# Optimization experiments

Hardware: AMD Instinct MI355X
Metric: run time of the kernel (lower is better)

Reference implementation:

```python
import jax, jax.numpy as jnp
import numpy as np

B, N, P, K, E = 4, 20000, 128, 128, 160000


def setup_inputs() -> dict:
    key = jax.random.key(0)
    ks = jax.random.split(key, 16)
    inv_p = 1.0 / np.sqrt(P)
    inv_3p = 1.0 / np.sqrt(3 * P)
    return {
        "x_in": jax.random.normal(ks[0], (B, N, P), jnp.float32),
        "vertex_areas": jax.random.uniform(ks[1], (B, N), jnp.float32, 1e-3, 1.0),
        "evals": jax.random.uniform(ks[2], (B, K), jnp.float32, 0.0, 10.0),
        "evecs": jax.random.normal(ks[3], (B, N, K), jnp.float32),
        "gradX_vals": jax.random.normal(ks[4], (B, E), jnp.float32),
        "gradY_vals": jax.random.normal(ks[5], (B, E), jnp.float32),
        "grad_rows": jax.random.randint(ks[6], (B, E), 0, N, jnp.int32),
        "grad_cols": jax.random.randint(ks[7], (B, E), 0, N, jnp.int32),
        # learned params
        "diffusion_times": jax.random.uniform(ks[8], (P,), jnp.float32, 1e-3, 0.1),
        "B_re": jax.random.normal(ks[9], (P, P), jnp.float32) * inv_p,
        "B_im": jax.random.normal(ks[10], (P, P), jnp.float32) * inv_p,
        "W1": jax.random.normal(ks[11], (P, 3 * P), jnp.float32) * inv_3p,
        "b1": jnp.zeros((P,), jnp.float32),
        "W2": jax.random.normal(ks[12], (P, P), jnp.float32) * inv_p,
        "b2": jnp.zeros((P,), jnp.float32),
        "W3": jax.random.normal(ks[13], (P, P), jnp.float32) * inv_p,
        "b3": jnp.zeros((P,), jnp.float32),
    }


def _spmm(rows, cols, vals, x):
    # sparse (n,n) @ dense (n,p) via COO gather/scatter
    return jax.ops.segment_sum(vals[:, None] * x[cols], rows, num_segments=x.shape[0])


def reference(x_in, vertex_areas, evals, evecs, gradX_vals, gradY_vals,
              grad_rows, grad_cols, diffusion_times, B_re, B_im,
              W1, b1, W2, b2, W3, b3):
    # SpectralDiffusion: project -> spectral heat scaling -> unproject
    times = jnp.clip(diffusion_times, 1e-8)                       # (P,)
    x_spec = jnp.einsum('bnk,bnp->bkp', evecs, x_in * vertex_areas[..., None])
    scale = jnp.exp(-evals[..., None] * times[None, None, :])     # (B,K,P)
    x_diffuse = jnp.einsum('bnk,bkp->bnp', evecs, scale * x_spec)  # (B,N,P)

    # sparse gradient halves
    gx = jax.vmap(_spmm)(grad_rows, grad_cols, gradX_vals, x_diffuse)  # (B,N,P)
    gy = jax.vmap(_spmm)(grad_rows, grad_cols, gradY_vals, x_diffuse)

    # SpatialGradient: tanh(re*B_re(re) + im*B_im(im))
    x_grad_features = jnp.tanh(gx * (gx @ B_re.T) + gy * (gy @ B_im.T))

    # MiniMLP on concatenated features (dropout inactive in eval)
    h = jnp.concatenate([x_in, x_diffuse, x_grad_features], axis=-1)  # (B,N,3P)
    h = jax.nn.relu(h @ W1.T + b1)
    h = jax.nn.relu(h @ W2.T + b2)
    h = h @ W3.T + b3
    return h + x_in
```

## Files before the change

### kernel.cpp

```cpp
#include <hip/hip_runtime.h>
#include <hip/hip_bf16.h>
#include <cstddef>

#define B_ 4
#define N_ 20000
#define P_ 128
#define K_ 128
#define E_ 160000

constexpr int NCH_S = 79;
constexpr int NSCB  = 79;

typedef __attribute__((ext_vector_type(8))) short short8;
typedef __attribute__((ext_vector_type(4))) float f32x4;

__device__ __forceinline__ unsigned pk2(float x, float y) {
  __hip_bfloat162 h = __float22bfloat162_rn(make_float2(x, y));
  union { __hip_bfloat162 h; unsigned u; } c; c.h = h; return c.u;
}
__device__ __forceinline__ float bf2f(short s) {
  union { unsigned u; float f; } c; c.u = ((unsigned)(unsigned short)s) << 16; return c.f;
}
__device__ __forceinline__ short f2bs(float x) {
  union { __hip_bfloat16 h; short s; } c; c.h = __float2bfloat16(x); return c.s;
}

__global__ __launch_bounds__(256)
void k_prep(const float* __restrict__ ev, const float* __restrict__ xin,
            const float* __restrict__ areas,
            __hip_bfloat16* __restrict__ evT, __hip_bfloat16* __restrict__ xT)
{
  const int tn = blockIdx.x, half = blockIdx.y & 1, mat = blockIdx.y >> 1;
  const int b = blockIdx.z, t = threadIdx.x;
  const int n0 = tn * 64, c0 = half * 64;
  __shared__ float ld[64][65];
  const float* src = (mat ? xin : ev) + (size_t)b * N_ * 128;
  const float* ab  = areas + (size_t)b * N_;
#pragma unroll
  for (int i = 0; i < 4; ++i) {
    int gid = t + i * 256;
    int r = gid >> 4, c4 = (gid & 15) << 2;
    int n = n0 + r;
    float4 v = make_float4(0.f, 0.f, 0.f, 0.f);
    if (n < N_) {
      v = *(const float4*)(src + (size_t)n * 128 + c0 + c4);
      if (mat == 0) { float ar = ab[n]; v.x *= ar; v.y *= ar; v.z *= ar; v.w *= ar; }
    }
    ld[r][c4] = v.x; ld[r][c4+1] = v.y; ld[r][c4+2] = v.z; ld[r][c4+3] = v.w;
  }
  __syncthreads();
  __hip_bfloat16* dst = (mat ? xT : evT) + (size_t)b * 128 * N_;
#pragma unroll
  for (int i = 0; i < 4; ++i) {
    int gid = t + i * 256;
    int cr = gid >> 4, nq = (gid & 15) << 2;
    int n = n0 + nq;
    if (n + 4 <= N_) {
      uint2 u;
      u.x = pk2(ld[nq][cr],   ld[nq+1][cr]);
      u.y = pk2(ld[nq+2][cr], ld[nq+3][cr]);
      *(uint2*)(dst + (size_t)(c0 + cr) * N_ + n) = u;
    }
  }
}

__global__ __launch_bounds__(256)
void k_wprep(const float* __restrict__ Bre, const float* __restrict__ Bim,
             uint4* __restrict__ WfRe, uint4* __restrict__ WfIm)
{
  int fid = blockIdx.x * 256 + threadIdx.x;
  if (fid >= 2048) return;
  int gg = fid >> 7, rr = fid & 127;
  const float* s0 = Bre + rr * 128 + gg * 8;
  const float* s1 = Bim + rr * 128 + gg * 8;
  float4 a0 = *(const float4*)s0, a1 = *(const float4*)(s0 + 4);
  uint4 u; u.x = pk2(a0.x, a0.y); u.y = pk2(a0.z, a0.w);
  u.z = pk2(a1.x, a1.y); u.w = pk2(a1.z, a1.w);
  WfRe[fid] = u;
  float4 b0 = *(const float4*)s1, b1 = *(const float4*)(s1 + 4);
  uint4 v; v.x = pk2(b0.x, b0.y); v.y = pk2(b0.z, b0.w);
  v.z = pk2(b1.x, b1.y); v.w = pk2(b1.z, b1.w);
  WfIm[fid] = v;
}

__device__ __forceinline__ void stg64(uint4* __restrict__ Ls,
                                      const __hip_bfloat16* __restrict__ G,
                                      int n0, int t)
{
#pragma unroll
  for (int i = 0; i < 2; ++i) {
    int gid = t + i * 512;
    int r = gid >> 3, kg = gid & 7;
    int n = n0 + kg * 8;
    uint4 u = make_uint4(0u, 0u, 0u, 0u);
    if (n < N_) u = *(const uint4*)(G + (size_t)r * N_ + n);
    Ls[r * 8 + (kg ^ (r & 7))] = u;
  }
}

__global__ __launch_bounds__(512)
void k_spec_mm(const __hip_bfloat16* __restrict__ evT,
               const __hip_bfloat16* __restrict__ xT,
               float* __restrict__ part)
{
  const int c = blockIdx.x, b = blockIdx.y, t = threadIdx.x;
  const int l = t & 63, wid = t >> 6;
  const int wr = wid >> 2, wc = wid & 3;
  const int lr = l & 15, lg = l >> 4;
  __shared__ uint4 AsB[1024];
  __shared__ uint4 WsB[1024];
  f32x4 acc[4][2];
#pragma unroll
  for (int m = 0; m < 4; ++m)
#pragma unroll
    for (int n = 0; n < 2; ++n) acc[m][n] = (f32x4)0.f;

  const __hip_bfloat16* eb = evT + (size_t)b * 128 * N_;
  const __hip_bfloat16* xb = xT  + (size_t)b * 128 * N_;

  for (int s = 0; s < 4; ++s) {
    int n0 = c * 256 + s * 64;
    __syncthreads();
    stg64(AsB, eb, n0, t);
    stg64(WsB, xb, n0, t);
    __syncthreads();
    const short8* Ap = (const short8*)AsB;
    const short8* Wp = (const short8*)WsB;
#pragma unroll
    for (int kk = 0; kk < 2; ++kk) {
      int gg = kk * 4 + lg;
      short8 a[4], w[2];
#pragma unroll
      for (int m = 0; m < 4; ++m) { int rr = wr*64 + m*16 + lr; a[m] = Ap[rr*8 + (gg ^ (rr & 7))]; }
#pragma unroll
      for (int n = 0; n < 2; ++n) { int rr = wc*32 + n*16 + lr; w[n] = Wp[rr*8 + (gg ^ (rr & 7))]; }
#pragma unroll
      for (int m = 0; m < 4; ++m)
#pragma unroll
        for (int n = 0; n < 2; ++n)
          acc[m][n] = __builtin_amdgcn_mfma_f32_16x16x32_bf16(a[m], w[n], acc[m][n], 0, 0, 0);
    }
  }

  float* po = part + ((size_t)(b * NCH_S + c) << 14);
#pragma unroll
  for (int m = 0; m < 4; ++m)
#pragma unroll
    for (int r = 0; r < 4; ++r) {
      int row = wr*64 + m*16 + lg*4 + r;
#pragma unroll
      for (int n = 0; n < 2; ++n) {
        int col = wc*32 + n*16 + lr;
        po[row * 128 + col] = acc[m][n][r];
      }
    }
}

__global__ __launch_bounds__(256)
void k_spec_reduce(const float* __restrict__ partial, const float* __restrict__ evals,
                   const float* __restrict__ times, float* __restrict__ sspecT)
{
  int idx = blockIdx.x * 256 + threadIdx.x;
  int b = idx >> 14;
  int kp = idx & 16383;
  int k = kp >> 7, p = kp & 127;
  float s = 0.f;
  const float* pb = partial + (size_t)b * NCH_S * (K_*P_) + kp;
  for (int c = 0; c < NCH_S; ++c) s += pb[(size_t)c * (K_*P_)];
  float tt = times[p]; tt = tt < 1e-8f ? 1e-8f : tt;
  float sc = __expf(-evals[b*K_ + k] * tt);
  sspecT[((size_t)b*P_ + p) * K_ + k] = s * sc;
}

__device__ __forceinline__ void stg_f32(uint4* __restrict__ Ls, const float* __restrict__ G,
                                        int ld, int nrows, int t)
{
#pragma unroll
  for (int i = 0; i < 4; ++i) {
    int gid = t + i * 512;
    int r = gid >> 4, kg = gid & 15;
    float4 v0 = make_float4(0.f,0.f,0.f,0.f), v1 = v0;
    if (r < nrows) {
      const float* p = G + (size_t)r * ld + kg * 8;
      v0 = *(const float4*)p;
      v1 = *(const float4*)(p + 4);
    }
    uint4 u;
    u.x = pk2(v0.x, v0.y); u.y = pk2(v0.z, v0.w);
    u.z = pk2(v1.x, v1.y); u.w = pk2(v1.z, v1.w);
    Ls[r * 16 + (kg ^ (r & 7))] = u;
  }
}

__device__ __forceinline__ void stg_bf(uint4* __restrict__ Ls,
                                       const __hip_bfloat16* __restrict__ G,
                                       int ld, int nrows, int t)
{
#pragma unroll
  for (int i = 0; i < 4; ++i) {
    int gid = t + i * 512;
    int r = gid >> 4, kg = gid & 15;
    uint4 u = make_uint4(0u,0u,0u,0u);
    if (r < nrows) u = *(const uint4*)(G + (size_t)r * ld + kg * 8);
    Ls[r * 16 + (kg ^ (r & 7))] = u;
  }
}

__device__ __forceinline__ void mfma_chunk(const uint4* AsB, const uint4* WsB,
                                           int wr, int wc, int lr, int lg,
                                           f32x4 acc[4][2])
{
  const short8* Ap = (const short8*)AsB;
  const short8* Wp = (const short8*)WsB;
#pragma unroll
  for (int kk = 0; kk < 4; ++kk) {
    int gg = kk * 4 + lg;
    short8 a[4], w[2];
#pragma unroll
    for (int m = 0; m < 4; ++m) {
      int rr = wr*64 + m*16 + lr;
      a[m] = Ap[rr*16 + (gg ^ (rr & 7))];
    }
#pragma unroll
    for (int n = 0; n < 2; ++n) {
      int rr = wc*32 + n*16 + lr;
      w[n] = Wp[rr*16 + (gg ^ (rr & 7))];
    }
#pragma unroll
    for (int m = 0; m < 4; ++m)
#pragma unroll
      for (int n = 0; n < 2; ++n)
        acc[m][n] = __builtin_amdgcn_mfma_f32_16x16x32_bf16(a[m], w[n], acc[m][n], 0, 0, 0);
  }
}

template<int MODE>
__global__ __launch_bounds__(512)
void k_rowgemm(const void* __restrict__ A0, const void* __restrict__ A1,
               const void* __restrict__ A2, int abf,
               const float* __restrict__ W, int ldw, int wbs, int nchunk,
               const float* __restrict__ bias, const float* __restrict__ resid,
               void* __restrict__ C)
{
  const int b = blockIdx.y, r0 = blockIdx.x * 128, t = threadIdx.x;
  const int l = t & 63, wid = t >> 6;
  const int wr = wid >> 2, wc = wid & 3;
  const int lr = l & 15, lg = l >> 4;
  __shared__ uint4 AsB[2048];
  __shared__ uint4 WsB[2048];
  f32x4 acc[4][2];
#pragma unroll
  for (int m = 0; m < 4; ++m)
#pragma unroll
    for (int n = 0; n < 2; ++n) acc[m][n] = (f32x4)0.f;

  const float* Wb = W + (size_t)b * wbs;
  const int nrows = min(128, N_ - r0);
  const size_t aoff = (size_t)b * N_ * 128 + (size_t)r0 * 128;

  for (int kc = 0; kc < nchunk; ++kc) {
    const void* Av = (kc == 0 ? A0 : (kc == 1 ? A1 : A2));
    __syncthreads();
    if ((abf >> kc) & 1) stg_bf(AsB, (const __hip_bfloat16*)Av + aoff, 128, nrows, t);
    else                 stg_f32(AsB, (const float*)Av + aoff, 128, nrows, t);
    stg_f32(WsB, Wb + kc * 128, ldw, 128, t);
    __syncthreads();
    mfma_chunk(AsB, WsB, wr, wc, lr, lg, acc);
  }

  const size_t cb = (size_t)b * N_ * 128;
#pragma unroll
  for (int m = 0; m < 4; ++m) {
    int rowt = wr*64 + m*16 + lg*4;
#pragma unroll
    for (int r = 0; r < 4; ++r) {
      int row = r0 + rowt + r;
      if (row >= N_) continue;
#pragma unroll
      for (int n = 0; n < 2; ++n) {
        int col = wc*32 + n*16 + lr;
        float v = acc[m][n][r];
        if (MODE == 1 || MODE == 2) v = fmaxf(v + bias[col], 0.f);
        if (MODE == 3) {
          v += bias[col] + resid[cb + (size_t)row*128 + col];
          ((float*)C)[cb + (size_t)row*128 + col] = v;
        } else {
          ((__hip_bfloat16*)C)[cb + (size_t)row*128 + col] = __float2bfloat16(v);
        }
      }
    }
  }
}

__device__ __forceinline__ void stg64r(uint4* __restrict__ Ls,
                                       const __hip_bfloat16* __restrict__ G,
                                       int nrows, int t)
{
#pragma unroll
  for (int i = 0; i < 4; ++i) {
    int gid = t + i * 256;
    int r = gid >> 4, kg = gid & 15;
    uint4 u = make_uint4(0u,0u,0u,0u);
    if (r < nrows) u = *(const uint4*)(G + (size_t)r * 128 + kg * 8);
    Ls[r * 16 + (kg ^ (r & 7))] = u;
  }
}

__device__ __forceinline__ void mfma_pass64(const uint4* As, const uint4* __restrict__ Wf,
                                            int wc, int lr, int lg, f32x4 acc[4][2])
{
  const short8* Ap = (const short8*)As;
  const short8* Wp = (const short8*)Wf;
#pragma unroll
  for (int kk = 0; kk < 4; ++kk) {
    int gg = kk * 4 + lg;
    short8 a[4], w[2];
#pragma unroll
    for (int m = 0; m < 4; ++m) { int rr = m*16 + lr; a[m] = Ap[rr*16 + (gg ^ (rr & 7))]; }
#pragma unroll
    for (int n = 0; n < 2; ++n) { int rr = wc*32 + n*16 + lr; w[n] = Wp[(gg << 7) + rr]; }
#pragma unroll
    for (int m = 0; m < 4; ++m)
#pragma unroll
      for (int n = 0; n < 2; ++n)
        acc[m][n] = __builtin_amdgcn_mfma_f32_16x16x32_bf16(a[m], w[n], acc[m][n], 0, 0, 0);
  }
}

__global__ __launch_bounds__(256)
void k_grad(const uint4* __restrict__ WfRe, const uint4* __restrict__ WfIm,
            __hip_bfloat16* __restrict__ gx, const __hip_bfloat16* __restrict__ gy)
{
  const int b = blockIdx.y, r0 = blockIdx.x * 64, t = threadIdx.x;
  const int l = t & 63, wc = t >> 6;
  const int lr = l & 15, lg = l >> 4;
  __shared__ uint4 As[1024];
  __shared__ uint4 As2[1024];
  f32x4 acc1[4][2], acc2[4][2];
#pragma unroll
  for (int m = 0; m < 4; ++m)
#pragma unroll
    for (int n = 0; n < 2; ++n) { acc1[m][n] = (f32x4)0.f; acc2[m][n] = (f32x4)0.f; }

  __hip_bfloat16*       gxb = gx + (size_t)b * N_ * P_;
  const __hip_bfloat16* gyb = gy + (size_t)b * N_ * P_;
  const int nrows = min(64, N_ - r0);

  stg64r(As,  gxb + (size_t)r0 * 128, nrows, t);
  stg64r(As2, gyb + (size_t)r0 * 128, nrows, t);
  __syncthreads();
  mfma_pass64(As,  WfRe, wc, lr, lg, acc1);
  mfma_pass64(As2, WfIm, wc, lr, lg, acc2);
  __syncthreads();

  short* S1 = (short*)As;
  short* S2 = (short*)As2;
#pragma unroll
  for (int m = 0; m < 4; ++m)
#pragma unroll
    for (int r = 0; r < 4; ++r) {
      int rowt = m*16 + lg*4 + r;
#pragma unroll
      for (int n = 0; n < 2; ++n) {
        int col = wc*32 + n*16 + lr;
        int idx = (rowt*16 + ((col>>3) ^ (rowt & 7)))*8 + (col & 7);
        S1[idx] = f2bs(acc1[m][n][r]);
        S2[idx] = f2bs(acc2[m][n][r]);
      }
    }
  __syncthreads();

  {
    const int row = t >> 2, cq = t & 3;
    if (row < nrows) {
      const short8* P1 = (const short8*)As;
      const short8* P2 = (const short8*)As2;
      const size_t gbase = (size_t)(r0 + row) * 128 + cq * 32;
#pragma unroll
      for (int cg = 0; cg < 4; ++cg) {
        int kg = cq * 4 + cg;
        short8 a1 = P1[row*16 + (kg ^ (row & 7))];
        short8 a2 = P2[row*16 + (kg ^ (row & 7))];
        uint4 ux = *(const uint4*)(gxb + gbase + cg*8);
        uint4 uy = *(const uint4*)(gyb + gbase + cg*8);
        unsigned xw[4] = {ux.x, ux.y, ux.z, ux.w};
        unsigned yw[4] = {uy.x, uy.y, uy.z, uy.w};
        unsigned ow[4];
#pragma unroll
        for (int p = 0; p < 4; ++p) {
          float g1l = __uint_as_float(xw[p] << 16);
          float g1h = __uint_as_float(xw[p] & 0xffff0000u);
          float g2l = __uint_as_float(yw[p] << 16);
          float g2h = __uint_as_float(yw[p] & 0xffff0000u);
          float sl = g1l * bf2f(a1[2*p])   + g2l * bf2f(a2[2*p]);
          float sh = g1h * bf2f(a1[2*p+1]) + g2h * bf2f(a2[2*p+1]);
          sl = fminf(fmaxf(sl, -15.f), 15.f);
          sh = fminf(fmaxf(sh, -15.f), 15.f);
          float el = __expf(2.f * sl), eh = __expf(2.f * sh);
          ow[p] = pk2((el - 1.f) / (el + 1.f), (eh - 1.f) / (eh + 1.f));
        }
        uint4 o; o.x = ow[0]; o.y = ow[1]; o.z = ow[2]; o.w = ow[3];
        *(uint4*)(gxb + gbase + cg*8) = o;
      }
    }
  }
}

__global__ void k_count(const int* __restrict__ rows, int* __restrict__ cnt)
{
  int b = blockIdx.y;
  int e = blockIdx.x * 256 + threadIdx.x;
  if (e < E_) atomicAdd(&cnt[b*N_ + rows[(size_t)b*E_ + e]], 1);
}

__global__ __launch_bounds__(256)
void k_scan_blk(const int* __restrict__ cnt, int* __restrict__ off,
                int* __restrict__ bsum)
{
  const int c = blockIdx.x, b = blockIdx.y, t = threadIdx.x;
  const int lane = t & 63, wid = t >> 6;
  __shared__ int wt[4];
  int i = c * 256 + t;
  int v = (i < N_) ? cnt[b*N_ + i] : 0;
  int x = v;
#pragma unroll
  for (int ofs = 1; ofs < 64; ofs <<= 1) {
    int y = __shfl_up(x, ofs, 64);
    if (lane >= ofs) x += y;
  }
  if (lane == 63) wt[wid] = x;
  __syncthreads();
  int wofs = 0;
  for (int wj = 0; wj < wid; ++wj) wofs += wt[wj];
  if (i < N_) off[b*(N_+1) + i] = wofs + x - v;
  if (t == 255) bsum[b*128 + c] = wofs + x;
}

__global__ __launch_bounds__(64)
void k_scan_top(int* __restrict__ bsum, int* __restrict__ off)
{
  const int b = blockIdx.x, t = threadIdx.x;
  int running = 0;
  for (int base = 0; base < 128; base += 64) {
    int i = base + t;
    int v = (i < NSCB) ? bsum[b*128 + i] : 0;
    int x = v;
#pragma unroll
    for (int ofs = 1; ofs < 64; ofs <<= 1) {
      int y = __shfl_up(x, ofs, 64);
      if (t >= ofs) x += y;
    }
    if (i < 128) bsum[b*128 + i] = running + x - v;
    running += __shfl(x, 63, 64);
  }
  if (t == 0) off[b*(N_+1) + N_] = running;
}

__global__ __launch_bounds__(256)
void k_scan_add(const int* __restrict__ bsum, int* __restrict__ off,
                int* __restrict__ pos)
{
  const int c = blockIdx.x, b = blockIdx.y;
  int i = c * 256 + (int)threadIdx.x;
  if (i < N_) {
    int o = off[b*(N_+1) + i] + bsum[b*128 + c];
    off[b*(N_+1) + i] = o;
    pos[b*N_ + i] = o;
  }
}

__global__ void k_fill(const int* __restrict__ rows, const int* __restrict__ cols,
                       const float* __restrict__ vx, const float* __restrict__ vy,
                       int* __restrict__ pos, uint4* __restrict__ prec)
{
  int b = blockIdx.y;
  int e = blockIdx.x * 256 + threadIdx.x;
  if (e < E_) {
    size_t be = (size_t)b*E_ + e;
    int r = rows[be];
    int p = atomicAdd(&pos[b*N_ + r], 1);
    if (p >= 0 && p < E_) {
      uint4 rec;
      rec.x = (unsigned)cols[be];
      rec.y = __float_as_uint(vx[be]);
      rec.z = __float_as_uint(vy[be]);
      rec.w = 0u;
      prec[(size_t)b*E_ + p] = rec;
    }
  }
}

__global__ __launch_bounds__(256)
void k_gather(const __hip_bfloat16* __restrict__ xd, const uint4* __restrict__ prec,
              const int* __restrict__ off,
              __hip_bfloat16* __restrict__ gx, __hip_bfloat16* __restrict__ gy)
{
  const int b = blockIdx.y;
  const int row = (blockIdx.x * 256 + threadIdx.x) >> 6;
  const int lane = threadIdx.x & 63;
  const int q = lane >> 4, ql = lane & 15;
  if (row >= N_) return;
  const int s = off[b*(N_+1) + row], e = off[b*(N_+1) + row + 1];
  float ax[8], ay[8];
#pragma unroll
  for (int k = 0; k < 8; ++k) { ax[k] = 0.f; ay[k] = 0.f; }
  const __hip_bfloat16* xdb = xd + (size_t)b * N_ * P_;
  const uint4* pb = prec + (size_t)b * E_;

  for (int i = s; i < e; i += 8) {
    int idx0 = i + q, idx1 = i + 4 + q;
    bool v0 = idx0 < e, v1 = idx1 < e;
    uint4 rec0 = pb[v0 ? idx0 : (e - 1)];
    uint4 rec1 = pb[v1 ? idx1 : (e - 1)];
    float fx0 = v0 ? __uint_as_float(rec0.y) : 0.f;
    float fy0 = v0 ? __uint_as_float(rec0.z) : 0.f;
    float fx1 = v1 ? __uint_as_float(rec1.y) : 0.f;
    float fy1 = v1 ? __uint_as_float(rec1.z) : 0.f;
    uint4 va = *(const uint4*)(xdb + (size_t)rec0.x * P_ + ql * 8);
    uint4 vb = *(const uint4*)(xdb + (size_t)rec1.x * P_ + ql * 8);
    unsigned aw[4] = {va.x, va.y, va.z, va.w};
    unsigned bw[4] = {vb.x, vb.y, vb.z, vb.w};
#pragma unroll
    for (int p = 0; p < 4; ++p) {
      float a_lo = __uint_as_float(aw[p] << 16);
      float a_hi = __uint_as_float(aw[p] & 0xffff0000u);
      float b_lo = __uint_as_float(bw[p] << 16);
      float b_hi = __uint_as_float(bw[p] & 0xffff0000u);
      ax[2*p]   = fmaf(fx0, a_lo, ax[2*p]);   ax[2*p]   = fmaf(fx1, b_lo, ax[2*p]);
      ax[2*p+1] = fmaf(fx0, a_hi, ax[2*p+1]); ax[2*p+1] = fmaf(fx1, b_hi, ax[2*p+1]);
      ay[2*p]   = fmaf(fy0, a_lo, ay[2*p]);   ay[2*p]   = fmaf(fy1, b_lo, ay[2*p]);
      ay[2*p+1] = fmaf(fy0, a_hi, ay[2*p+1]); ay[2*p+1] = fmaf(fy1, b_hi, ay[2*p+1]);
    }
  }
#pragma unroll
  for (int k = 0; k < 8; ++k) {
    ax[k] += __shfl_xor(ax[k], 16, 64); ax[k] += __shfl_xor(ax[k], 32, 64);
    ay[k] += __shfl_xor(ay[k], 16, 64); ay[k] += __shfl_xor(ay[k], 32, 64);
  }
  if (lane < 16) {
    size_t o = (size_t)b * N_ * P_ + (size_t)row * P_ + ql * 8;
    uint4 ux, uy;
    ux.x = pk2(ax[0], ax[1]); ux.y = pk2(ax[2], ax[3]);
    ux.z = pk2(ax[4], ax[5]); ux.w = pk2(ax[6], ax[7]);
    uy.x = pk2(ay[0], ay[1]); uy.y = pk2(ay[2], ay[3]);
    uy.z = pk2(ay[4], ay[5]); uy.w = pk2(ay[6], ay[7]);
    *(uint4*)(gx + o) = ux;
    *(uint4*)(gy + o) = uy;
  }
}

extern "C" void kernel_launch(void* const* d_in, const int* in_sizes, int n_in,
                              void* d_out, int out_size, void* d_ws, size_t ws_size,
                              hipStream_t stream)
{
  const float* x_in  = (const float*)d_in[0];
  const float* areas = (const float*)d_in[1];
  const float* evals = (const float*)d_in[2];
  const float* evecs = (const float*)d_in[3];
  const float* gXv   = (const float*)d_in[4];
  const float* gYv   = (const float*)d_in[5];
  const int*   grows = (const int*)d_in[6];
  const int*   gcols = (const int*)d_in[7];
  const float* times = (const float*)d_in[8];
  const float* Bre   = (const float*)d_in[9];
  const float* Bim   = (const float*)d_in[10];
  const float* W1    = (const float*)d_in[11];
  const float* b1    = (const float*)d_in[12];
  const float* W2    = (const float*)d_in[13];
  const float* b2    = (const float*)d_in[14];
  const float* W3    = (const float*)d_in[15];
  const float* b3    = (const float*)d_in[16];

  float* ws = (float*)d_ws;
  __hip_bfloat16* xd_bf = (__hip_bfloat16*)ws;
  float*          part  = ws + 6000000;
  __hip_bfloat16* gx_bf = (__hip_bfloat16*)(ws + 12000000);
  __hip_bfloat16* gy_bf = (__hip_bfloat16*)(ws + 18000000);
  __hip_bfloat16* evT   = gx_bf;
  __hip_bfloat16* xT    = gy_bf;

  uint4* prec   = (uint4*)(ws + 24000000);
  int*   ipos   = (int*)(ws + 26560000);
  int*   ioff   = ipos + B_*N_;
  float* sspecT = ws + 26750000;
  uint4* WfRe   = (uint4*)(ws + 26816000);
  uint4* WfIm   = WfRe + 2048;
  int*   bsum   = (int*)(WfIm + 2048);
  float* out    = (float*)d_out;

  const int GB = (N_ + 127) / 128;
  const int TN = (N_ + 63) / 64;

  k_prep<<<dim3(TN, 4, B_), 256, 0, stream>>>(evecs, x_in, areas, evT, xT);
  k_wprep<<<dim3(8), 256, 0, stream>>>(Bre, Bim, WfRe, WfIm);
  k_spec_mm<<<dim3(NCH_S, B_), 512, 0, stream>>>(evT, xT, part);
  k_spec_reduce<<<dim3(B_*K_*P_/256), 256, 0, stream>>>(part, evals, times, sspecT);
  k_rowgemm<0><<<dim3(GB, B_), 512, 0, stream>>>(evecs, nullptr, nullptr, 0, sspecT,
                                                 128, K_*P_, 1, nullptr, nullptr, xd_bf);
  hipMemsetAsync(ipos, 0, (size_t)B_*N_*sizeof(int), stream);
  k_count<<<dim3(E_/256, B_), 256, 0, stream>>>(grows, ipos);
  k_scan_blk<<<dim3(NSCB, B_), 256, 0, stream>>>(ipos, ioff, bsum);
  k_scan_top<<<dim3(B_), 64, 0, stream>>>(bsum, ioff);
  k_scan_add<<<dim3(NSCB, B_), 256, 0, stream>>>(bsum, ioff, ipos);
  k_fill<<<dim3(E_/256, B_), 256, 0, stream>>>(grows, gcols, gXv, gYv, ipos, prec);
  k_gather<<<dim3(N_/4, B_), 256, 0, stream>>>(xd_bf, prec, ioff, gx_bf, gy_bf);
  k_grad<<<dim3(TN, B_), 256, 0, stream>>>(WfRe, WfIm, gx_bf, gy_bf);
  k_rowgemm<1><<<dim3(GB, B_), 512, 0, stream>>>(x_in, xd_bf, gx_bf, 0b110, W1,
                                                 384, 0, 3, b1, nullptr, gy_bf);
  k_rowgemm<2><<<dim3(GB, B_), 512, 0, stream>>>(gy_bf, nullptr, nullptr, 1, W2,
                                                 128, 0, 1, b2, nullptr, gx_bf);
  k_rowgemm<3><<<dim3(GB, B_), 512, 0, stream>>>(gx_bf, nullptr, nullptr, 1, W3,
                                                 128, 0, 1, b3, x_in, out);
}
```

Measured before the change: 261.2 us.

## Fuse three MLP GEMMs into one kernel and pre-pack weights to bf16

Replaces the three separate row-GEMM launches of the MLP with a single kernel that keeps each 64-row tile's intermediate activations in shared memory across all three layers, adding bias, ReLU and the residual in place. Weights (W1/W2/W3 and the spectral scale matrix) are converted to swizzled bf16 fragments once by small prep kernels instead of every block re-converting fp32 weights into LDS. The unprojection GEMM also switches to the 64-row kernel structure with pre-packed weights. This removes intermediate global round-trips and redundant weight conversion, at the cost of extra LDS syncs and smaller tiles per block.

```diff
diff --git a/kernel.cpp b/kernel.cpp
--- a/kernel.cpp
+++ b/kernel.cpp
@@ -83,6 +83,40 @@
   WfIm[fid] = v;
 }
 
+__global__ __launch_bounds__(256)
+void k_wprep_mlp(const float* __restrict__ W1, const float* __restrict__ W2,
+                 const float* __restrict__ W3, uint4* __restrict__ W1f,
+                 uint4* __restrict__ W2f, uint4* __restrict__ W3f)
+{
+  int fid = blockIdx.x * 256 + threadIdx.x;
+  if (fid >= 10240) return;
+  int j = fid >> 11, wi = fid & 2047;
+  int gg = wi >> 7, rr = wi & 127;
+  const float* src;
+  uint4* dst;
+  if (j < 3)      { src = W1 + rr * 384 + j * 128 + gg * 8; dst = W1f + j * 2048 + wi; }
+  else if (j == 3){ src = W2 + rr * 128 + gg * 8;           dst = W2f + wi; }
+  else            { src = W3 + rr * 128 + gg * 8;           dst = W3f + wi; }
+  float4 a0 = *(const float4*)src, a1 = *(const float4*)(src + 4);
+  uint4 u; u.x = pk2(a0.x, a0.y); u.y = pk2(a0.z, a0.w);
+  u.z = pk2(a1.x, a1.y); u.w = pk2(a1.z, a1.w);
+  *dst = u;
+}
+
+__global__ __launch_bounds__(256)
+void k_wprep_spec(const float* __restrict__ sspecT, uint4* __restrict__ sTf)
+{
+  int fid = blockIdx.x * 256 + threadIdx.x;
+  if (fid >= 8192) return;
+  int b = fid >> 11, wi = fid & 2047;
+  int gg = wi >> 7, p = wi & 127;
+  const float* src = sspecT + ((size_t)b * P_ + p) * K_ + gg * 8;
+  float4 a0 = *(const float4*)src, a1 = *(const float4*)(src + 4);
+  uint4 u; u.x = pk2(a0.x, a0.y); u.y = pk2(a0.z, a0.w);
+  u.z = pk2(a1.x, a1.y); u.w = pk2(a1.z, a1.w);
+  sTf[(size_t)b * 2048 + wi] = u;
+}
+
 __device__ __forceinline__ void stg64(uint4* __restrict__ Ls,
                                       const __hip_bfloat16* __restrict__ G,
                                       int n0, int t)
@@ -172,126 +206,6 @@
   sspecT[((size_t)b*P_ + p) * K_ + k] = s * sc;
 }
 
-__device__ __forceinline__ void stg_f32(uint4* __restrict__ Ls, const float* __restrict__ G,
-                                        int ld, int nrows, int t)
-{
-#pragma unroll
-  for (int i = 0; i < 4; ++i) {
-    int gid = t + i * 512;
-    int r = gid >> 4, kg = gid & 15;
-    float4 v0 = make_float4(0.f,0.f,0.f,0.f), v1 = v0;
-    if (r < nrows) {
-      const float* p = G + (size_t)r * ld + kg * 8;
-      v0 = *(const float4*)p;
-      v1 = *(const float4*)(p + 4);
-    }
-    uint4 u;
-    u.x = pk2(v0.x, v0.y); u.y = pk2(v0.z, v0.w);
-    u.z = pk2(v1.x, v1.y); u.w = pk2(v1.z, v1.w);
-    Ls[r * 16 + (kg ^ (r & 7))] = u;
-  }
-}
-
-__device__ __forceinline__ void stg_bf(uint4* __restrict__ Ls,
-                                       const __hip_bfloat16* __restrict__ G,
-                                       int ld, int nrows, int t)
-{
-#pragma unroll
-  for (int i = 0; i < 4; ++i) {
-    int gid = t + i * 512;
-    int r = gid >> 4, kg = gid & 15;
-    uint4 u = make_uint4(0u,0u,0u,0u);
-    if (r < nrows) u = *(const uint4*)(G + (size_t)r * ld + kg * 8);
-    Ls[r * 16 + (kg ^ (r & 7))] = u;
-  }
-}
-
-__device__ __forceinline__ void mfma_chunk(const uint4* AsB, const uint4* WsB,
-                                           int wr, int wc, int lr, int lg,
-                                           f32x4 acc[4][2])
-{
-  const short8* Ap = (const short8*)AsB;
-  const short8* Wp = (const short8*)WsB;
-#pragma unroll
-  for (int kk = 0; kk < 4; ++kk) {
-    int gg = kk * 4 + lg;
-    short8 a[4], w[2];
-#pragma unroll
-    for (int m = 0; m < 4; ++m) {
-      int rr = wr*64 + m*16 + lr;
-      a[m] = Ap[rr*16 + (gg ^ (rr & 7))];
-    }
-#pragma unroll
-    for (int n = 0; n < 2; ++n) {
-      int rr = wc*32 + n*16 + lr;
-      w[n] = Wp[rr*16 + (gg ^ (rr & 7))];
-    }
-#pragma unroll
-    for (int m = 0; m < 4; ++m)
-#pragma unroll
-      for (int n = 0; n < 2; ++n)
-        acc[m][n] = __builtin_amdgcn_mfma_f32_16x16x32_bf16(a[m], w[n], acc[m][n], 0, 0, 0);
-  }
-}
-
-template<int MODE>
-__global__ __launch_bounds__(512)
-void k_rowgemm(const void* __restrict__ A0, const void* __restrict__ A1,
-               const void* __restrict__ A2, int abf,
-               const float* __restrict__ W, int ldw, int wbs, int nchunk,
-               const float* __restrict__ bias, const float* __restrict__ resid,
-               void* __restrict__ C)
-{
-  const int b = blockIdx.y, r0 = blockIdx.x * 128, t = threadIdx.x;
-  const int l = t & 63, wid = t >> 6;
-  const int wr = wid >> 2, wc = wid & 3;
-  const int lr = l & 15, lg = l >> 4;
-  __shared__ uint4 AsB[2048];
-  __shared__ uint4 WsB[2048];
-  f32x4 acc[4][2];
-#pragma unroll
-  for (int m = 0; m < 4; ++m)
-#pragma unroll
-    for (int n = 0; n < 2; ++n) acc[m][n] = (f32x4)0.f;
-
-  const float* Wb = W + (size_t)b * wbs;
-  const int nrows = min(128, N_ - r0);
-  const size_t aoff = (size_t)b * N_ * 128 + (size_t)r0 * 128;
-
-  for (int kc = 0; kc < nchunk; ++kc) {
-    const void* Av = (kc == 0 ? A0 : (kc == 1 ? A1 : A2));
-    __syncthreads();
-    if ((abf >> kc) & 1) stg_bf(AsB, (const __hip_bfloat16*)Av + aoff, 128, nrows, t);
-    else                 stg_f32(AsB, (const float*)Av + aoff, 128, nrows, t);
-    stg_f32(WsB, Wb + kc * 128, ldw, 128, t);
-    __syncthreads();
-    mfma_chunk(AsB, WsB, wr, wc, lr, lg, acc);
-  }
-
-  const size_t cb = (size_t)b * N_ * 128;
-#pragma unroll
-  for (int m = 0; m < 4; ++m) {
-    int rowt = wr*64 + m*16 + lg*4;
-#pragma unroll
-    for (int r = 0; r < 4; ++r) {
-      int row = r0 + rowt + r;
-      if (row >= N_) continue;
-#pragma unroll
-      for (int n = 0; n < 2; ++n) {
-        int col = wc*32 + n*16 + lr;
-        float v = acc[m][n][r];
-        if (MODE == 1 || MODE == 2) v = fmaxf(v + bias[col], 0.f);
-        if (MODE == 3) {
-          v += bias[col] + resid[cb + (size_t)row*128 + col];
-          ((float*)C)[cb + (size_t)row*128 + col] = v;
-        } else {
-          ((__hip_bfloat16*)C)[cb + (size_t)row*128 + col] = __float2bfloat16(v);
-        }
-      }
-    }
-  }
-}
-
 __device__ __forceinline__ void stg64r(uint4* __restrict__ Ls,
                                        const __hip_bfloat16* __restrict__ G,
                                        int nrows, int t)
@@ -306,6 +220,27 @@
   }
 }
 
+__device__ __forceinline__ void stg64r_f32(uint4* __restrict__ Ls,
+                                           const float* __restrict__ G,
+                                           int nrows, int t)
+{
+#pragma unroll
+  for (int i = 0; i < 4; ++i) {
+    int gid = t + i * 256;
+    int r = gid >> 4, kg = gid & 15;
+    float4 v0 = make_float4(0.f,0.f,0.f,0.f), v1 = v0;
+    if (r < nrows) {
+      const float* p = G + (size_t)r * 128 + kg * 8;
+      v0 = *(const float4*)p;
+      v1 = *(const float4*)(p + 4);
+    }
+    uint4 u;
+    u.x = pk2(v0.x, v0.y); u.y = pk2(v0.z, v0.w);
+    u.z = pk2(v1.x, v1.y); u.w = pk2(v1.z, v1.w);
+    Ls[r * 16 + (kg ^ (r & 7))] = u;
+  }
+}
+
 __device__ __forceinline__ void mfma_pass64(const uint4* As, const uint4* __restrict__ Wf,
                                             int wc, int lr, int lg, f32x4 acc[4][2])
 {
@@ -325,6 +260,38 @@
       for (int n = 0; n < 2; ++n)
         acc[m][n] = __builtin_amdgcn_mfma_f32_16x16x32_bf16(a[m], w[n], acc[m][n], 0, 0, 0);
   }
+}
+
+__global__ __launch_bounds__(256)
+void k_unproj(const float* __restrict__ evecs, const uint4* __restrict__ sTf,
+              __hip_bfloat16* __restrict__ xd)
+{
+  const int b = blockIdx.y, r0 = blockIdx.x * 64, t = threadIdx.x;
+  const int l = t & 63, w = t >> 6;
+  const int lr = l & 15, lg = l >> 4;
+  __shared__ uint4 LA[1024];
+  f32x4 acc[4][2];
+#pragma unroll
+  for (int m = 0; m < 4; ++m)
+#pragma unroll
+    for (int n = 0; n < 2; ++n) acc[m][n] = (f32x4)0.f;
+  const int nrows = min(64, N_ - r0);
+  stg64r_f32(LA, evecs + (size_t)b * N_ * 128 + (size_t)r0 * 128, nrows, t);
+  __syncthreads();
+  mfma_pass64(LA, sTf + (size_t)b * 2048, w, lr, lg, acc);
+  __hip_bfloat16* xdb = xd + (size_t)b * N_ * P_;
+#pragma unroll
+  for (int m = 0; m < 4; ++m)
+#pragma unroll
+    for (int r = 0; r < 4; ++r) {
+      int row = r0 + m*16 + lg*4 + r;
+      if (row >= N_) continue;
+#pragma unroll
+      for (int n = 0; n < 2; ++n) {
+        int col = w*32 + n*16 + lr;
+        xdb[(size_t)row*128 + col] = __float2bfloat16(acc[m][n][r]);
+      }
+    }
 }
 
 __global__ __launch_bounds__(256)
@@ -401,6 +368,124 @@
         }
         uint4 o; o.x = ow[0]; o.y = ow[1]; o.z = ow[2]; o.w = ow[3];
         *(uint4*)(gxb + gbase + cg*8) = o;
+      }
+    }
+  }
+}
+
+__global__ __launch_bounds__(256)
+void k_mlp(const float* __restrict__ xin, const __hip_bfloat16* __restrict__ xd,
+           const __hip_bfloat16* __restrict__ xg,
+           const uint4* __restrict__ W1f, const uint4* __restrict__ W2f,
+           const uint4* __restrict__ W3f,
+           const float* __restrict__ b1, const float* __restrict__ b2,
+           const float* __restrict__ b3, float* __restrict__ out)
+{
+  const int b = blockIdx.y, r0 = blockIdx.x * 64, t = threadIdx.x;
+  const int l = t & 63, w = t >> 6;
+  const int lr = l & 15, lg = l >> 4;
+  __shared__ uint4 LA[1024];
+  __shared__ uint4 LB[1024];
+  const int nrows = min(64, N_ - r0);
+  const float* xinb = xin + (size_t)b * N_ * 128 + (size_t)r0 * 128;
+
+  f32x4 acc[4][2];
+#pragma unroll
+  for (int m = 0; m < 4; ++m)
+#pragma unroll
+    for (int n = 0; n < 2; ++n) acc[m][n] = (f32x4)0.f;
+
+  for (int kc = 0; kc < 3; ++kc) {
+    __syncthreads();
+    if (kc == 0)      stg64r_f32(LA, xinb, nrows, t);
+    else if (kc == 1) stg64r(LA, xd + (size_t)b * N_ * 128 + (size_t)r0 * 128, nrows, t);
+    else              stg64r(LA, xg + (size_t)b * N_ * 128 + (size_t)r0 * 128, nrows, t);
+    __syncthreads();
+    mfma_pass64(LA, W1f + kc * 2048, w, lr, lg, acc);
+  }
+  {
+    float bb[2] = { b1[w*32 + lr], b1[w*32 + 16 + lr] };
+    short* Sh = (short*)LB;
+#pragma unroll
+    for (int m = 0; m < 4; ++m)
+#pragma unroll
+      for (int r = 0; r < 4; ++r) {
+        int rowt = m*16 + lg*4 + r;
+#pragma unroll
+        for (int n = 0; n < 2; ++n) {
+          int col = w*32 + n*16 + lr;
+          float v = fmaxf(acc[m][n][r] + bb[n], 0.f);
+          Sh[(rowt*16 + ((col>>3) ^ (rowt & 7)))*8 + (col & 7)] = f2bs(v);
+        }
+      }
+  }
+  __syncthreads();
+
+#pragma unroll
+  for (int m = 0; m < 4; ++m)
+#pragma unroll
+    for (int n = 0; n < 2; ++n) acc[m][n] = (f32x4)0.f;
+  mfma_pass64(LB, W2f, w, lr, lg, acc);
+  __syncthreads();
+  {
+    float bb[2] = { b2[w*32 + lr], b2[w*32 + 16 + lr] };
+    short* Sh = (short*)LB;
+#pragma unroll
+    for (int m = 0; m < 4; ++m)
+#pragma unroll
+      for (int r = 0; r < 4; ++r) {
+        int rowt = m*16 + lg*4 + r;
+#pragma unroll
+        for (int n = 0; n < 2; ++n) {
+          int col = w*32 + n*16 + lr;
+          float v = fmaxf(acc[m][n][r] + bb[n], 0.f);
+          Sh[(rowt*16 + ((col>>3) ^ (rowt & 7)))*8 + (col & 7)] = f2bs(v);
+        }
+      }
+  }
+  __syncthreads();
+
+#pragma unroll
+  for (int m = 0; m < 4; ++m)
+#pragma unroll
+    for (int n = 0; n < 2; ++n) acc[m][n] = (f32x4)0.f;
+  mfma_pass64(LB, W3f, w, lr, lg, acc);
+  __syncthreads();
+
+  {
+    float bb[2] = { b3[w*32 + lr], b3[w*32 + 16 + lr] };
+    float* F1 = (float*)LA;
+    float* F2 = (float*)LB;
+#pragma unroll
+    for (int m = 0; m < 4; ++m)
+#pragma unroll
+      for (int r = 0; r < 4; ++r) {
+        int rowt = m*16 + lg*4 + r;
+#pragma unroll
+        for (int n = 0; n < 2; ++n) {
+          int col = w*32 + n*16 + lr;
+          float v = acc[m][n][r] + bb[n];
+          if (col < 64) F1[rowt*64 + col] = v;
+          else          F2[rowt*64 + col - 64] = v;
+        }
+      }
+  }
+  __syncthreads();
+
+  {
+    const int row = t >> 2, cq = t & 3;
+    if (row < nrows) {
+      const float* Fs = (cq < 2) ? (const float*)LA : (const float*)LB;
+      const float* fbase = Fs + row*64 + (cq & 1)*32;
+      const float* xr = xinb + (size_t)row * 128 + cq * 32;
+      float* orow = out + (size_t)b * N_ * 128 + (size_t)(r0 + row) * 128 + cq * 32;
+#pragma unroll
+      for (int j = 0; j < 8; ++j) {
+        float4 s = ((const float4*)fbase)[j];
+        float4 xv = ((const float4*)xr)[j];
+        float4 o; o.x = s.x + xv.x; o.y = s.y + xv.y;
+        o.z = s.z + xv.z; o.w = s.w + xv.w;
+        ((float4*)orow)[j] = o;
       }
     }
   }
@@ -586,17 +671,21 @@
   uint4* WfRe   = (uint4*)(ws + 26816000);
   uint4* WfIm   = WfRe + 2048;
   int*   bsum   = (int*)(WfIm + 2048);
+  uint4* W1f    = (uint4*)(ws + 26834000);
+  uint4* W2f    = W1f + 6144;
+  uint4* W3f    = W2f + 2048;
+  uint4* sTf    = W3f + 2048;
   float* out    = (float*)d_out;
 
-  const int GB = (N_ + 127) / 128;
   const int TN = (N_ + 63) / 64;
 
   k_prep<<<dim3(TN, 4, B_), 256, 0, stream>>>(evecs, x_in, areas, evT, xT);
   k_wprep<<<dim3(8), 256, 0, stream>>>(Bre, Bim, WfRe, WfIm);
+  k_wprep_mlp<<<dim3(40), 256, 0, stream>>>(W1, W2, W3, W1f, W2f, W3f);
   k_spec_mm<<<dim3(NCH_S, B_), 512, 0, stream>>>(evT, xT, part);
   k_spec_reduce<<<dim3(B_*K_*P_/256), 256, 0, stream>>>(part, evals, times, sspecT);
-  k_rowgemm<0><<<dim3(GB, B_), 512, 0, stream>>>(evecs, nullptr, nullptr, 0, sspecT,
-                                                 128, K_*P_, 1, nullptr, nullptr, xd_bf);
+  k_wprep_spec<<<dim3(32), 256, 0, stream>>>(sspecT, sTf);
+  k_unproj<<<dim3(TN, B_), 256, 0, stream>>>(evecs, sTf, xd_bf);
   hipMemsetAsync(ipos, 0, (size_t)B_*N_*sizeof(int), stream);
   k_count<<<dim3(E_/256, B_), 256, 0, stream>>>(grows, ipos);
   k_scan_blk<<<dim3(NSCB, B_), 256, 0, stream>>>(ipos, ioff, bsum);
@@ -605,10 +694,6 @@
   k_fill<<<dim3(E_/256, B_), 256, 0, stream>>>(grows, gcols, gXv, gYv, ipos, prec);
   k_gather<<<dim3(N_/4, B_), 256, 0, stream>>>(xd_bf, prec, ioff, gx_bf, gy_bf);
   k_grad<<<dim3(TN, B_), 256, 0, stream>>>(WfRe, WfIm, gx_bf, gy_bf);
-  k_rowgemm<1><<<dim3(GB, B_), 512, 0, stream>>>(x_in, xd_bf, gx_bf, 0b110, W1,
-                                                 384, 0, 3, b1, nullptr, gy_bf);
-  k_rowgemm<2><<<dim3(GB, B_), 512, 0, stream>>>(gy_bf, nullptr, nullptr, 1, W2,
-                                                 128, 0, 1, b2, nullptr, gx_bf);
-  k_rowgemm<3><<<dim3(GB, B_), 512, 0, stream>>>(gx_bf, nullptr, nullptr, 1, W3,
-                                                 128, 0, 1, b3, x_in, out);
-}
+  k_mlp<<<dim3(TN, B_), 256, 0, stream>>>(x_in, xd_bf, gx_bf, W1f, W2f, W3f,
+                                          b1, b2, b3, out);
+}
```

New measurement: 238.5 us, median of 3. 1.1x faster.
